# Kernel tuning notes

Measured on AMD Instinct MI355X. Metric: run time of the kernel, lower is better.

The kernel has to match this reference:

```python
import jax, jax.numpy as jnp
import numpy as np

B = 4096      # batch
N = 8192      # feature dim (sorted axis)
K_SPARSE = 512


def setup_inputs() -> dict:
    key = jax.random.key(0)
    x = jax.random.normal(key, (B, N), dtype=jnp.float32)
    return {"x": x, "k": K_SPARSE}


def reference(x, k):
    # Train-phase branch of KSparse.call:
    #   kth_smallest = sort(x)[..., N-1-k]  (the (k+1)-th largest value per row)
    #   out = x * (x > kth_smallest[:, None])
    n = x.shape[-1]
    kth = jnp.sort(x, axis=-1)[..., n - 1 - k]          # [B]
    mask = (x > kth[..., None]).astype(x.dtype)          # strictly greater -> keeps top-k
    return x * mask
```

## Files before the change

### kernel.cpp

```cpp
#include <hip/hip_runtime.h>

#define NTHREADS 512
#define N_FEAT   8192
#define EPT      (N_FEAT / NTHREADS)
#define NB0      4096
#define CAP      2048

typedef float f4v __attribute__((ext_vector_type(4)));

__device__ __forceinline__ unsigned f2k(float f) {
    unsigned u = __float_as_uint(f);
    return u ^ (unsigned)(((int)u >> 31) | 0x80000000);
}
__device__ __forceinline__ float k2f(unsigned kk) {
    return __uint_as_float(kk ^ (unsigned)(((int)(~kk) >> 31) | 0x80000000));
}

__global__ __launch_bounds__(NTHREADS) void ksparse_kernel(
    const float* __restrict__ x, const int* __restrict__ kptr,
    float* __restrict__ out) {

    const int t    = threadIdx.x;
    const int lane = t & 63;
    const int w    = t >> 6;
    const size_t base = (size_t)blockIdx.x * N_FEAT;

    __shared__ unsigned hist[NB0];
    __shared__ unsigned cand[CAP];
    __shared__ unsigned ws[8];
    __shared__ unsigned s_bucket, s_r, s_cnt, s_kth;

    const f4v* xv = (const f4v*)(x + base);
    f4v v0 = xv[t], v1 = xv[t + 512], v2 = xv[t + 1024], v3 = xv[t + 1536];

#pragma unroll
    for (int i = 0; i < NB0 / NTHREADS; ++i) hist[t + i * NTHREADS] = 0u;
    if (t == 0) s_cnt = 0u;
    __syncthreads();

    unsigned key[EPT];
#pragma unroll
    for (int j = 0; j < 4; ++j) {
        key[0 + j] = f2k(v0[j]);
        key[4 + j] = f2k(v1[j]);
        key[8 + j] = f2k(v2[j]);
        key[12 + j] = f2k(v3[j]);
    }

    const unsigned r = (unsigned)kptr[0] + 1u;

#pragma unroll
    for (int i = 0; i < EPT; ++i) {
        unsigned b = key[i] >> 20;
        atomicAdd(&hist[((b & 7u) << 9) | (b >> 3)], 1u);
    }
    __syncthreads();

    unsigned h[8], sum8 = 0;
#pragma unroll
    for (int j = 0; j < 8; ++j) { h[j] = hist[(j << 9) | t]; sum8 += h[j]; }
    unsigned S = sum8;
#pragma unroll
    for (int off = 1; off < 64; off <<= 1) {
        unsigned q = (unsigned)__shfl_down((int)S, off, 64);
        if (lane + off < 64) S += q;
    }
    if (lane == 0) ws[w] = S;
    __syncthreads();
    unsigned above = S - sum8;
#pragma unroll
    for (int w2 = 0; w2 < 8; ++w2) if (w2 > w) above += ws[w2];
    if (above < r && above + sum8 >= r) {
        unsigned acc = above;
#pragma unroll
        for (int j = 7; j >= 0; --j) {
            if (acc < r && acc + h[j] >= r) { s_bucket = (unsigned)(8 * t + j); s_r = r - acc; }
            acc += h[j];
        }
    }
    __syncthreads();
    const unsigned bucket = s_bucket;
    const unsigned r2 = s_r;

#pragma unroll
    for (int i = 0; i < EPT; ++i) {
        if ((key[i] >> 20) == bucket) {
            unsigned p = atomicAdd(&s_cnt, 1u);
            if (p < CAP) cand[p] = key[i];
        }
    }
    __syncthreads();
    const unsigned m = s_cnt;

    if (m <= CAP) {
        for (unsigned i = t; i < m; i += NTHREADS) {
            unsigned ki = cand[i], g = 0, ge = 0;
            for (unsigned j = 0; j < m; ++j) {
                unsigned kj = cand[j];
                g  += (kj > ki);
                ge += (kj >= ki);
            }
            if (g < r2 && ge >= r2) s_kth = ki;
        }
    } else {
        unsigned prefix = bucket << 20;
        unsigned rr = r2;
        for (int pass = 0; pass < 2; ++pass) {
            const int shift = (pass == 0) ? 10 : 0;
            const unsigned hm = (pass == 0) ? 0xFFF00000u : 0xFFFFFC00u;
            hist[t] = 0u; hist[t + 512] = 0u;
            __syncthreads();
            for (int i = 0; i < EPT; ++i)
                if ((key[i] & hm) == prefix)
                    atomicAdd(&hist[(key[i] >> shift) & 1023u], 1u);
            __syncthreads();
            if (t < 64) {
                const unsigned* hb = hist + t * 16;
                unsigned C = 0;
                for (int j2 = 0; j2 < 16; ++j2) C += hb[j2];
                unsigned S2 = C;
                for (int off = 1; off < 64; off <<= 1) {
                    unsigned q = (unsigned)__shfl_down((int)S2, off, 64);
                    if (lane + off < 64) S2 += q;
                }
                unsigned carry = S2 - C;
                if (S2 >= rr && carry < rr) {
                    unsigned acc = carry;
                    for (int j2 = 15; j2 >= 0; --j2) {
                        unsigned ge2 = acc + hb[j2];
                        if (acc < rr && ge2 >= rr) { s_bucket = (unsigned)(t * 16 + j2); s_r = rr - acc; }
                        acc = ge2;
                    }
                }
            }
            __syncthreads();
            prefix |= s_bucket << shift;
            rr = s_r;
        }
        if (t == 0) s_kth = prefix;
    }
    __syncthreads();
    const unsigned kth = s_kth;

    f4v* ov = (f4v*)(out + base);
#pragma unroll
    for (int i = 0; i < 4; ++i) {
        f4v o;
#pragma unroll
        for (int j = 0; j < 4; ++j) {
            unsigned kk = key[4 * i + j];
            o[j] = (kk > kth) ? k2f(kk) : 0.0f;
        }
        __builtin_nontemporal_store(o, ov + t + i * NTHREADS);
    }
}

extern "C" void kernel_launch(void* const* d_in, const int* in_sizes, int n_in,
                              void* d_out, int out_size, void* d_ws, size_t ws_size,
                              hipStream_t stream) {
    const float* x = (const float*)d_in[0];
    const int* k   = (const int*)d_in[1];
    float* out     = (float*)d_out;
    const int B = in_sizes[0] / N_FEAT;
    ksparse_kernel<<<B, NTHREADS, 0, stream>>>(x, k, out);
}
```

Measured before the change: 52.32 us.

## Process four rows per block with next-row prefetch and padded histogram

Each block now handles four rows in turn, loading the next row's data into registers while the current row's histogram select runs. The aim is to hide global-load latency and spread block setup cost over several rows. The histogram layout changes to a padded linear index to avoid bank conflicts, and the final mask compares floats directly instead of keys. In exchange the grid shrinks to a quarter of the blocks, which may lower occupancy and parallelism across CUs, and register pressure rises from holding two rows at once.

```diff
diff --git a/kernel.cpp b/kernel.cpp
--- a/kernel.cpp
+++ b/kernel.cpp
@@ -2,9 +2,10 @@
 
 #define NTHREADS 512
 #define N_FEAT   8192
-#define EPT      (N_FEAT / NTHREADS)
 #define NB0      4096
+#define SKSZ     (NB0 + NB0 / 8)
 #define CAP      2048
+#define ROWS     4
 
 typedef float f4v __attribute__((ext_vector_type(4)));
 
@@ -18,140 +19,166 @@
 
 __global__ __launch_bounds__(NTHREADS) void ksparse_kernel(
     const float* __restrict__ x, const int* __restrict__ kptr,
-    float* __restrict__ out) {
+    float* __restrict__ out, int nrows) {
 
     const int t    = threadIdx.x;
     const int lane = t & 63;
     const int w    = t >> 6;
-    const size_t base = (size_t)blockIdx.x * N_FEAT;
 
-    __shared__ unsigned hist[NB0];
+    __shared__ unsigned hist[SKSZ];
     __shared__ unsigned cand[CAP];
     __shared__ unsigned ws[8];
-    __shared__ unsigned s_bucket, s_r, s_cnt, s_kth;
+    __shared__ unsigned s_bucket, s_r, s_kth;
+    __shared__ unsigned s_cnt[2];
 
-    const f4v* xv = (const f4v*)(x + base);
-    f4v v0 = xv[t], v1 = xv[t + 512], v2 = xv[t + 1024], v3 = xv[t + 1536];
+    const int row0 = blockIdx.x * ROWS;
+    const size_t rowbase = (size_t)row0 * N_FEAT;
+    const f4v* xv = (const f4v*)(x + rowbase);
+    f4v* ov = (f4v*)(out + rowbase);
+
+    f4v c0 = xv[t], c1 = xv[t + 512], c2 = xv[t + 1024], c3 = xv[t + 1536];
 
 #pragma unroll
-    for (int i = 0; i < NB0 / NTHREADS; ++i) hist[t + i * NTHREADS] = 0u;
-    if (t == 0) s_cnt = 0u;
+    for (int i = 0; i < SKSZ / NTHREADS; ++i) hist[t + i * NTHREADS] = 0u;
+    if (t == 0) { s_cnt[0] = 0u; s_cnt[1] = 0u; }
     __syncthreads();
-
-    unsigned key[EPT];
-#pragma unroll
-    for (int j = 0; j < 4; ++j) {
-        key[0 + j] = f2k(v0[j]);
-        key[4 + j] = f2k(v1[j]);
-        key[8 + j] = f2k(v2[j]);
-        key[12 + j] = f2k(v3[j]);
-    }
 
     const unsigned r = (unsigned)kptr[0] + 1u;
 
+    for (int rr = 0; rr < ROWS; ++rr) {
+        if (row0 + rr >= nrows) break;
+        const int p = rr & 1;
+
+        f4v n0, n1, n2, n3;
+        if (rr + 1 < ROWS && row0 + rr + 1 < nrows) {
+            const f4v* nv = xv + (size_t)(rr + 1) * (N_FEAT / 4);
+            n0 = nv[t]; n1 = nv[t + 512]; n2 = nv[t + 1024]; n3 = nv[t + 1536];
+        }
+
+        {
+            auto h4 = [&](f4v v) {
 #pragma unroll
-    for (int i = 0; i < EPT; ++i) {
-        unsigned b = key[i] >> 20;
-        atomicAdd(&hist[((b & 7u) << 9) | (b >> 3)], 1u);
-    }
-    __syncthreads();
+                for (int j = 0; j < 4; ++j) {
+                    unsigned b = f2k(v[j]) >> 20;
+                    atomicAdd(&hist[b + (b >> 3)], 1u);
+                }
+            };
+            h4(c0); h4(c1); h4(c2); h4(c3);
+        }
+        __syncthreads();
 
-    unsigned h[8], sum8 = 0;
+        unsigned h[8], sum8 = 0;
 #pragma unroll
-    for (int j = 0; j < 8; ++j) { h[j] = hist[(j << 9) | t]; sum8 += h[j]; }
-    unsigned S = sum8;
+        for (int j = 0; j < 8; ++j) { h[j] = hist[9 * t + j]; sum8 += h[j]; }
+        unsigned S = sum8;
 #pragma unroll
-    for (int off = 1; off < 64; off <<= 1) {
-        unsigned q = (unsigned)__shfl_down((int)S, off, 64);
-        if (lane + off < 64) S += q;
-    }
-    if (lane == 0) ws[w] = S;
-    __syncthreads();
-    unsigned above = S - sum8;
+        for (int off = 1; off < 64; off <<= 1) {
+            unsigned q = (unsigned)__shfl_down((int)S, off, 64);
+            if (lane + off < 64) S += q;
+        }
+        if (lane == 0) ws[w] = S;
+        __syncthreads();
+        unsigned above = S - sum8;
 #pragma unroll
-    for (int w2 = 0; w2 < 8; ++w2) if (w2 > w) above += ws[w2];
-    if (above < r && above + sum8 >= r) {
-        unsigned acc = above;
+        for (int w2 = 1; w2 < 8; ++w2) if (w2 > w) above += ws[w2];
+        if (above < r && above + sum8 >= r) {
+            unsigned acc = above;
 #pragma unroll
-        for (int j = 7; j >= 0; --j) {
-            if (acc < r && acc + h[j] >= r) { s_bucket = (unsigned)(8 * t + j); s_r = r - acc; }
-            acc += h[j];
+            for (int j = 7; j >= 0; --j) {
+                if (acc < r && acc + h[j] >= r) { s_bucket = (unsigned)(8 * t + j); s_r = r - acc; }
+                acc += h[j];
+            }
         }
-    }
-    __syncthreads();
-    const unsigned bucket = s_bucket;
-    const unsigned r2 = s_r;
+        __syncthreads();
+        const unsigned bucket = s_bucket;
+        const unsigned r2 = s_r;
 
+        {
+            auto g4 = [&](f4v v) {
 #pragma unroll
-    for (int i = 0; i < EPT; ++i) {
-        if ((key[i] >> 20) == bucket) {
-            unsigned p = atomicAdd(&s_cnt, 1u);
-            if (p < CAP) cand[p] = key[i];
-        }
-    }
-    __syncthreads();
-    const unsigned m = s_cnt;
-
-    if (m <= CAP) {
-        for (unsigned i = t; i < m; i += NTHREADS) {
-            unsigned ki = cand[i], g = 0, ge = 0;
-            for (unsigned j = 0; j < m; ++j) {
-                unsigned kj = cand[j];
-                g  += (kj > ki);
-                ge += (kj >= ki);
-            }
-            if (g < r2 && ge >= r2) s_kth = ki;
-        }
-    } else {
-        unsigned prefix = bucket << 20;
-        unsigned rr = r2;
-        for (int pass = 0; pass < 2; ++pass) {
-            const int shift = (pass == 0) ? 10 : 0;
-            const unsigned hm = (pass == 0) ? 0xFFF00000u : 0xFFFFFC00u;
-            hist[t] = 0u; hist[t + 512] = 0u;
-            __syncthreads();
-            for (int i = 0; i < EPT; ++i)
-                if ((key[i] & hm) == prefix)
-                    atomicAdd(&hist[(key[i] >> shift) & 1023u], 1u);
-            __syncthreads();
-            if (t < 64) {
-                const unsigned* hb = hist + t * 16;
-                unsigned C = 0;
-                for (int j2 = 0; j2 < 16; ++j2) C += hb[j2];
-                unsigned S2 = C;
-                for (int off = 1; off < 64; off <<= 1) {
-                    unsigned q = (unsigned)__shfl_down((int)S2, off, 64);
-                    if (lane + off < 64) S2 += q;
-                }
-                unsigned carry = S2 - C;
-                if (S2 >= rr && carry < rr) {
-                    unsigned acc = carry;
-                    for (int j2 = 15; j2 >= 0; --j2) {
-                        unsigned ge2 = acc + hb[j2];
-                        if (acc < rr && ge2 >= rr) { s_bucket = (unsigned)(t * 16 + j2); s_r = rr - acc; }
-                        acc = ge2;
+                for (int j = 0; j < 4; ++j) {
+                    unsigned kk = f2k(v[j]);
+                    if ((kk >> 20) == bucket) {
+                        unsigned q = atomicAdd(&s_cnt[p], 1u);
+                        if (q < CAP) cand[q] = kk;
                     }
                 }
+            };
+            g4(c0); g4(c1); g4(c2); g4(c3);
+        }
+#pragma unroll
+        for (int i = 0; i < SKSZ / NTHREADS; ++i) hist[t + i * NTHREADS] = 0u;
+        if (t == 0) s_cnt[p ^ 1] = 0u;
+        __syncthreads();
+        const unsigned m = s_cnt[p];
+
+        if (m <= CAP) {
+            for (unsigned i = t; i < m; i += NTHREADS) {
+                unsigned ki = cand[i], g = 0, ge = 0;
+                for (unsigned j2 = 0; j2 < m; ++j2) {
+                    unsigned kj = cand[j2];
+                    g  += (kj > ki);
+                    ge += (kj >= ki);
+                }
+                if (g < r2 && ge >= r2) s_kth = ki;
             }
-            __syncthreads();
-            prefix |= s_bucket << shift;
-            rr = s_r;
+        } else {
+            unsigned prefix = bucket << 20, rk = r2;
+            for (int pass = 0; pass < 2; ++pass) {
+                const int shift = pass == 0 ? 10 : 0;
+                const unsigned hm = pass == 0 ? 0xFFF00000u : 0xFFFFFC00u;
+                auto a4 = [&](f4v v) {
+#pragma unroll
+                    for (int j = 0; j < 4; ++j) {
+                        unsigned kk = f2k(v[j]);
+                        if ((kk & hm) == prefix) atomicAdd(&hist[(kk >> shift) & 1023u], 1u);
+                    }
+                };
+                a4(c0); a4(c1); a4(c2); a4(c3);
+                __syncthreads();
+                if (t < 64) {
+                    unsigned C = 0, hh[16];
+#pragma unroll
+                    for (int j2 = 0; j2 < 16; ++j2) { hh[j2] = hist[t * 16 + j2]; C += hh[j2]; }
+                    unsigned S2 = C;
+#pragma unroll
+                    for (int off = 1; off < 64; off <<= 1) {
+                        unsigned q = (unsigned)__shfl_down((int)S2, off, 64);
+                        if (lane + off < 64) S2 += q;
+                    }
+                    unsigned carry = S2 - C;
+                    if (S2 >= rk && carry < rk) {
+                        unsigned acc = carry;
+#pragma unroll
+                        for (int j2 = 15; j2 >= 0; --j2) {
+                            if (acc < rk && acc + hh[j2] >= rk) { s_bucket = (unsigned)(t * 16 + j2); s_r = rk - acc; }
+                            acc += hh[j2];
+                        }
+                    }
+                }
+                __syncthreads();
+                prefix |= s_bucket << shift;
+                rk = s_r;
+                hist[t] = 0u; hist[t + 512] = 0u;
+                __syncthreads();
+            }
+            if (t == 0) s_kth = prefix;
         }
-        if (t == 0) s_kth = prefix;
-    }
-    __syncthreads();
-    const unsigned kth = s_kth;
+        __syncthreads();
+        const float kthf = k2f(s_kth);
 
-    f4v* ov = (f4v*)(out + base);
+        f4v* orow = ov + (size_t)rr * (N_FEAT / 4);
+        {
+            auto w4 = [&](f4v v, int idx) {
+                f4v o;
 #pragma unroll
-    for (int i = 0; i < 4; ++i) {
-        f4v o;
-#pragma unroll
-        for (int j = 0; j < 4; ++j) {
-            unsigned kk = key[4 * i + j];
-            o[j] = (kk > kth) ? k2f(kk) : 0.0f;
+                for (int j = 0; j < 4; ++j) o[j] = (v[j] > kthf) ? v[j] : 0.0f;
+                __builtin_nontemporal_store(o, orow + idx);
+            };
+            w4(c0, t); w4(c1, t + 512); w4(c2, t + 1024); w4(c3, t + 1536);
         }
-        __builtin_nontemporal_store(o, ov + t + i * NTHREADS);
+
+        c0 = n0; c1 = n1; c2 = n2; c3 = n3;
     }
 }
 
@@ -162,5 +189,6 @@
     const int* k   = (const int*)d_in[1];
     float* out     = (float*)d_out;
     const int B = in_sizes[0] / N_FEAT;
-    ksparse_kernel<<<B, NTHREADS, 0, stream>>>(x, k, out);
+    const int grid = (B + ROWS - 1) / ROWS;
+    ksparse_kernel<<<grid, NTHREADS, 0, stream>>>(x, k, out, B);
 }
```

Measured after the change: 87.43 us. 1.67x slower.
